# Optimization experiments

Measured on AMD Instinct MI355X. Metric: run time of the kernel, lower is better.

## Reference

```python
import jax, jax.numpy as jnp
import numpy as np

B, O, E, D, H = 8192, 64, 16, 16, 4  # batch, num_orbital, num_electron, n_bf_dets, hidden


def setup_inputs() -> dict:
    key = jax.random.key(0)
    ks = jax.random.split(key, 6)
    # occupation vectors: exactly E ones among O orbitals per sample
    scores = jax.random.uniform(ks[0], (B, O))
    occ_idx = jnp.argsort(scores, axis=1)[:, :E]  # (B, E) random occupied positions
    x = jnp.zeros((B, O), jnp.float32).at[jnp.arange(B)[:, None], occ_idx].set(1.0)
    # hidden MLP (positive_random_init kernels, zero bias as in flax default)
    W1 = jax.random.uniform(ks[1], (O, H), jnp.float32, minval=1.0, maxval=1.1)
    b1 = jnp.zeros((H,), jnp.float32)
    W2 = jax.random.uniform(ks[2], (H, H), jnp.float32, minval=1.0, maxval=1.1)
    b2 = jnp.zeros((H,), jnp.float32)
    # DenseGeneral: H -> (D, O, E)
    Wg = jax.random.normal(ks[3], (H, D, O, E), jnp.float32) / np.float32(np.sqrt(H))
    bg = jnp.zeros((D, O, E), jnp.float32)
    # bf_det_params: lecun_normal on (D, 1)
    bf_det_params = jax.random.normal(ks[4], (D, 1), jnp.float32) / np.float32(np.sqrt(D))
    return dict(x=x, W1=W1, b1=b1, W2=W2, b2=b2, Wg=Wg, bg=bg,
                bf_det_params=bf_det_params)


def reference(x, W1, b1, W2, b2, Wg, bg, bf_det_params):
    num_e = Wg.shape[-1]
    # indices of first num_e nonzero orbitals per sample (fill 0, like jnp.nonzero size=)
    sel = jax.vmap(lambda r: jnp.nonzero(r, size=num_e, fill_value=0)[0])(x)  # (B, E)
    # tiny MLP with relu
    h = jax.nn.relu(x @ W1 + b1)          # (B, H)
    h = jax.nn.relu(h @ W2 + b2)          # (B, H)
    # DenseGeneral projection to (B, D, O, E)
    y = jnp.einsum('bh,hdoe->bdoe', h, Wg) + bg
    # gather occupied-orbital rows -> (B, D, E, E)
    g = jax.vmap(lambda yi, si: yi[:, si, :])(y, sel)
    dets = jnp.linalg.det(g)              # (B, D)
    out = (dets @ bf_det_params)[:, 0]    # (B,)
    # zero out samples whose selected indices sum to 0 (empty/degenerate config)
    return jnp.where(jnp.sum(sel, axis=1) == 0, jnp.float32(0.0), out)
```

## Files before the change

### kernel.cpp

```cpp
#include <hip/hip_runtime.h>


template <int CTRL>
__device__ __forceinline__ float dpp_movf(float v) {
    return __int_as_float(__builtin_amdgcn_update_dpp(
        0, __float_as_int(v), CTRL, 0xF, 0xF, true));
}

__global__ __launch_bounds__(64) void backflow_kernel(
    const float* __restrict__ x,
    const float* __restrict__ W1,
    const float* __restrict__ b1,
    const float* __restrict__ W2,
    const float* __restrict__ b2,
    const float* __restrict__ Wg,
    const float* __restrict__ bg,
    const float* __restrict__ bf,
    float* __restrict__ out,
    int B)
{
    const int lane = threadIdx.x;
    const int b    = blockIdx.x;
    if (b >= B) return;
    const int d = lane >> 2;
    const int l = lane & 3;

    __shared__ float4 smem[512];

    const float xv = x[b * 64 + lane];
    const unsigned long long mask = __ballot(xv != 0.0f);
    const bool empty = ((mask & ~1ull) == 0ull);

    const float4 w1 = reinterpret_cast<const float4*>(W1)[lane];
    float c0 = xv * w1.x, c1 = xv * w1.y, c2 = xv * w1.z, c3 = xv * w1.w;
    #pragma unroll
    for (int off = 32; off >= 1; off >>= 1) {
        c0 += __shfl_xor(c0, off);
        c1 += __shfl_xor(c1, off);
        c2 += __shfl_xor(c2, off);
        c3 += __shfl_xor(c3, off);
    }
    const float h10 = fmaxf(c0 + b1[0], 0.0f);
    const float h11 = fmaxf(c1 + b1[1], 0.0f);
    const float h12 = fmaxf(c2 + b1[2], 0.0f);
    const float h13 = fmaxf(c3 + b1[3], 0.0f);

    float h2[4];
    #pragma unroll
    for (int j = 0; j < 4; ++j) {
        float v = b2[j];
        v = fmaf(h10, W2[0 * 4 + j], v);
        v = fmaf(h11, W2[1 * 4 + j], v);
        v = fmaf(h12, W2[2 * 4 + j], v);
        v = fmaf(h13, W2[3 * 4 + j], v);
        h2[j] = fmaxf(v, 0.0f);
    }

    unsigned long long mr = mask;
    #pragma unroll
    for (int i = 0; i < 15; ++i) if (i < d) mr &= mr - 1;
    const int selr = mr ? (int)__builtin_ctzll(mr) : 0;

    float R0[16], R1[16], R2[16], R3[16];

    {
        const float4* wgp = reinterpret_cast<const float4*>(Wg);
        const float4* bgp = reinterpret_cast<const float4*>(bg);
        const int rowoff = selr * 4 + l;

        #pragma unroll 1
        for (int half = 0; half < 2; ++half) {
            #pragma unroll 1
            for (int dd = 0; dd < 8; ++dd) {
                const int ds = half * 8 + dd;
                const float4 wb  = bgp[ds * 256 + rowoff];
                const float4 w3  = wgp[(3 * 16 + ds) * 256 + rowoff];
                const float4 w2c = wgp[(2 * 16 + ds) * 256 + rowoff];
                const float4 wv1 = wgp[(1 * 16 + ds) * 256 + rowoff];
                const float4 w0  = wgp[(0 * 16 + ds) * 256 + rowoff];
                float4 a;
                a.x = fmaf(h2[0],w0.x, fmaf(h2[1],wv1.x, fmaf(h2[2],w2c.x, fmaf(h2[3],w3.x, wb.x))));
                a.y = fmaf(h2[0],w0.y, fmaf(h2[1],wv1.y, fmaf(h2[2],w2c.y, fmaf(h2[3],w3.y, wb.y))));
                a.z = fmaf(h2[0],w0.z, fmaf(h2[1],wv1.z, fmaf(h2[2],w2c.z, fmaf(h2[3],w3.z, wb.z))));
                a.w = fmaf(h2[0],w0.w, fmaf(h2[1],wv1.w, fmaf(h2[2],w2c.w, fmaf(h2[3],w3.w, wb.w))));
                smem[(ds & 7) * 64 + d * 4 + (l ^ (ds & 3))] = a;
                __builtin_amdgcn_sched_barrier(0);
            }
            __syncthreads();
            if ((d >> 3) == half) {
#define RD_ROWS(RW, S) do { _Pragma("unroll")                                 \
                for (int q = 0; q < 4; ++q) {                                 \
                    const float4 t = smem[(d & 7) * 64 + (l + 4 * (S)) * 4 + (q ^ (d & 3))]; \
                    RW[q*4+0] = t.x; RW[q*4+1] = t.y;                         \
                    RW[q*4+2] = t.z; RW[q*4+3] = t.w;                         \
                } } while (0)
                RD_ROWS(R0, 0);
                RD_ROWS(R1, 1);
                RD_ROWS(R2, 2);
                RD_ROWS(R3, 3);
#undef RD_ROWS
            }
            __syncthreads();
        }
    }

#define BUILD_ROW(RW, SQ) do {                                                   \
    const float* base = Wg + ((size_t)d * 64 + (SQ)) * 16;                       \
    const float4* p0 = reinterpret_cast<const float4*>(base);                    \
    const float4* p1 = reinterpret_cast<const float4*>(base + 16384);            \
    const float4* p2 = reinterpret_cast<const float4*>(base + 32768);            \
    const float4* p3 = reinterpret_cast<const float4*>(base + 49152);            \
    const float4* pb = reinterpret_cast<const float4*>(bg + ((size_t)d * 64 + (SQ)) * 16); \
    _Pragma("unroll")                                                            \
    for (int q = 0; q < 4; ++q) {                                                \
        const float4 a0 = p0[q], a1 = p1[q], a2 = p2[q], a3 = p3[q], ab = pb[q]; \
        RW[q*4+0] = fmaf(h2[0],a0.x, fmaf(h2[1],a1.x, fmaf(h2[2],a2.x, fmaf(h2[3],a3.x, ab.x)))); \
        RW[q*4+1] = fmaf(h2[0],a0.y, fmaf(h2[1],a1.y, fmaf(h2[2],a2.y, fmaf(h2[3],a3.y, ab.y)))); \
        RW[q*4+2] = fmaf(h2[0],a0.z, fmaf(h2[1],a1.z, fmaf(h2[2],a2.z, fmaf(h2[3],a3.z, ab.z)))); \
        RW[q*4+3] = fmaf(h2[0],a0.w, fmaf(h2[1],a1.w, fmaf(h2[2],a2.w, fmaf(h2[3],a3.w, ab.w)))); \
    } } while (0)

    float mm = 0.0f;
    #pragma unroll
    for (int j = 0; j < 16; ++j) {
        mm = fmaxf(mm, fmaxf(fmaxf(fabsf(R0[j]), fabsf(R1[j])),
                             fmaxf(fabsf(R2[j]), fabsf(R3[j]))));
    }
    mm = fmaxf(mm, dpp_movf<0xB1>(mm));
    mm = fmaxf(mm, dpp_movf<0x4E>(mm));
    const float tau = 1e-4f * mm;

#define STEP4(K, DAC, PA, PB, PC, PD) do {                                   \
        const float pivot = dpp_movf<((K) & 3) * 0x55>(PA[0]);               \
        nb += !(fabsf(pivot) >= tau);                                        \
        DAC *= (double)pivot;                                                \
        const float pinv = __builtin_amdgcn_rcpf(pivot);                     \
        const float fa = (l > ((K) & 3)) ? PA[0] * pinv : 0.0f;              \
        const float fb = PB[0] * pinv;                                       \
        const float fc = PC[0] * pinv;                                       \
        const float fd = PD[0] * pinv;                                       \
        _Pragma("unroll")                                                    \
        for (int j = 1; j <= 15 - (K); ++j) {                                \
            const float pv = dpp_movf<((K) & 3) * 0x55>(PA[j]);              \
            PA[j - 1] = fmaf(-fa, pv, PA[j]);                                \
            PB[j - 1] = fmaf(-fb, pv, PB[j]);                                \
            PC[j - 1] = fmaf(-fc, pv, PC[j]);                                \
            PD[j - 1] = fmaf(-fd, pv, PD[j]);                                \
        } } while (0)

#define STEP3(K, DAC, PA, PB, PC) do {                                       \
        const float pivot = dpp_movf<((K) & 3) * 0x55>(PA[0]);               \
        nb += !(fabsf(pivot) >= tau);                                        \
        DAC *= (double)pivot;                                                \
        const float pinv = __builtin_amdgcn_rcpf(pivot);                     \
        const float fa = (l > ((K) & 3)) ? PA[0] * pinv : 0.0f;              \
        const float fb = PB[0] * pinv;                                       \
        const float fc = PC[0] * pinv;                                       \
        _Pragma("unroll")                                                    \
        for (int j = 1; j <= 15 - (K); ++j) {                                \
            const float pv = dpp_movf<((K) & 3) * 0x55>(PA[j]);              \
            PA[j - 1] = fmaf(-fa, pv, PA[j]);                                \
            PB[j - 1] = fmaf(-fb, pv, PB[j]);                                \
            PC[j - 1] = fmaf(-fc, pv, PC[j]);                                \
        } } while (0)

#define STEP2(K, DAC, PA, PB) do {                                           \
        const float pivot = dpp_movf<((K) & 3) * 0x55>(PA[0]);               \
        nb += !(fabsf(pivot) >= tau);                                        \
        DAC *= (double)pivot;                                                \
        const float pinv = __builtin_amdgcn_rcpf(pivot);                     \
        const float fa = (l > ((K) & 3)) ? PA[0] * pinv : 0.0f;              \
        const float fb = PB[0] * pinv;                                       \
        _Pragma("unroll")                                                    \
        for (int j = 1; j <= 15 - (K); ++j) {                                \
            const float pv = dpp_movf<((K) & 3) * 0x55>(PA[j]);              \
            PA[j - 1] = fmaf(-fa, pv, PA[j]);                                \
            PB[j - 1] = fmaf(-fb, pv, PB[j]);                                \
        } } while (0)

#define STEP1(K, DAC, PA) do {                                               \
        const float pivot = dpp_movf<((K) & 3) * 0x55>(PA[0]);               \
        nb += !(fabsf(pivot) >= tau);                                        \
        DAC *= (double)pivot;                                                \
        const float pinv = __builtin_amdgcn_rcpf(pivot);                     \
        const float fa = (l > ((K) & 3)) ? PA[0] * pinv : 0.0f;              \
        _Pragma("unroll")                                                    \
        for (int j = 1; j <= 15 - (K); ++j) {                                \
            const float pv = dpp_movf<((K) & 3) * 0x55>(PA[j]);              \
            PA[j - 1] = fmaf(-fa, pv, PA[j]);                                \
        } } while (0)

    double deta, detb;
    bool   retried = false;

    #pragma unroll 1
    for (int attempt = 0; attempt < 2; ++attempt) {
        if (attempt) {
            unsigned long long m = mask;
            if (l & 1) { m &= m - 1; }
            if (l & 2) { m &= m - 1; m &= m - 1; }
            const int s0 = m ? (int)__builtin_ctzll(m) : 0;
            m &= m - 1; m &= m - 1; m &= m - 1; m &= m - 1;
            const int s1 = m ? (int)__builtin_ctzll(m) : 0;
            m &= m - 1; m &= m - 1; m &= m - 1; m &= m - 1;
            const int s2 = m ? (int)__builtin_ctzll(m) : 0;
            m &= m - 1; m &= m - 1; m &= m - 1; m &= m - 1;
            const int s3 = m ? (int)__builtin_ctzll(m) : 0;
            BUILD_ROW(R0, s0);
            BUILD_ROW(R1, s1);
            BUILD_ROW(R2, s2);
            BUILD_ROW(R3, s3);
            const bool z = (l == 0);
            #pragma unroll
            for (int j = 0; j < 16; ++j) {
                const float w0 = z ? R1[j] : R0[j];
                const float wv = z ? R2[j] : R1[j];
                const float w2 = z ? R3[j] : R2[j];
                const float w3 = z ? R0[j] : R3[j];
                R0[j] = fmaf(0.5f, dpp_movf<0x39>(w0), R0[j]);
                R1[j] = fmaf(0.5f, dpp_movf<0x39>(wv), R1[j]);
                R2[j] = fmaf(0.5f, dpp_movf<0x39>(w2), R2[j]);
                R3[j] = fmaf(0.5f, dpp_movf<0x39>(w3), R3[j]);
            }
            retried = true;
        }
        deta = 1.0; detb = 1.0;
        int nb = 0;

        STEP4(0,  deta, R0, R1, R2, R3);
        STEP4(1,  detb, R0, R1, R2, R3);
        STEP4(2,  deta, R0, R1, R2, R3);
        STEP4(3,  detb, R0, R1, R2, R3);
        STEP3(4,  deta, R1, R2, R3);
        STEP3(5,  detb, R1, R2, R3);
        STEP3(6,  deta, R1, R2, R3);
        STEP3(7,  detb, R1, R2, R3);
        STEP2(8,  deta, R2, R3);
        STEP2(9,  detb, R2, R3);
        STEP2(10, deta, R2, R3);
        STEP2(11, detb, R2, R3);
        STEP1(12, deta, R3);
        STEP1(13, detb, R3);
        STEP1(14, deta, R3);
        STEP1(15, detb, R3);

        if (nb == 0) break;
    }
#undef STEP1
#undef STEP2
#undef STEP3
#undef STEP4
#undef BUILD_ROW

    float detf = (float)(deta * detb);
    if (retried) detf *= (65536.0f / 65535.0f);
    float acc = (l == 0) ? detf * bf[d] : 0.0f;
    acc += __shfl_xor(acc, 4);
    acc += __shfl_xor(acc, 8);
    acc += __shfl_xor(acc, 16);
    acc += __shfl_xor(acc, 32);
    if (lane == 0) out[b] = empty ? 0.0f : acc;
}

extern "C" void kernel_launch(void* const* d_in, const int* in_sizes, int n_in,
                              void* d_out, int out_size, void* d_ws, size_t ws_size,
                              hipStream_t stream) {
    const float* x  = (const float*)d_in[0];
    const float* W1 = (const float*)d_in[1];
    const float* b1 = (const float*)d_in[2];
    const float* W2 = (const float*)d_in[3];
    const float* b2 = (const float*)d_in[4];
    const float* Wg = (const float*)d_in[5];
    const float* bg = (const float*)d_in[6];
    const float* bf = (const float*)d_in[7];
    float* out = (float*)d_out;

    const int B = in_sizes[0] / 64;
    backflow_kernel<<<B, 64, 0, stream>>>(x, W1, b1, W2, b2, Wg, bg, bf, out, B);
}
```

Baseline: 46.16 us.

## Pack eight samples per block and share double-buffered Wg slices in LDS

The kernel now runs 8 waves per 512-thread block, one sample per wave. Each determinant slice of Wg and bg is loaded cooperatively into double-buffered shared memory and reused by all 8 waves, instead of every sample issuing its own scattered global gathers. The retry path is reorganised so the whole wave retries but only determinants that failed the pivot test apply the mixing and scale factor. This adds a block-wide barrier per slice and more shared memory, and drops the b>=B guard, so it assumes B is a multiple of 8.

```diff
diff --git a/kernel.cpp b/kernel.cpp
--- a/kernel.cpp
+++ b/kernel.cpp
@@ -7,7 +7,7 @@
         0, __float_as_int(v), CTRL, 0xF, 0xF, true));
 }
 
-__global__ __launch_bounds__(64) void backflow_kernel(
+__global__ __launch_bounds__(512) void backflow_kernel(
     const float* __restrict__ x,
     const float* __restrict__ W1,
     const float* __restrict__ b1,
@@ -19,13 +19,15 @@
     float* __restrict__ out,
     int B)
 {
-    const int lane = threadIdx.x;
-    const int b    = blockIdx.x;
-    if (b >= B) return;
+    const int lane  = threadIdx.x & 63;
+    const int wavei = threadIdx.x >> 6;
+    const int b     = blockIdx.x * 8 + wavei;
     const int d = lane >> 2;
     const int l = lane & 3;
 
-    __shared__ float4 smem[512];
+    __shared__ float4 slice[2][1280];
+    __shared__ float4 Bm[8][64];
+    float4* const bm = Bm[wavei];
 
     const float xv = x[b * 64 + lane];
     const unsigned long long mask = __ballot(xv != 0.0f);
@@ -60,47 +62,70 @@
     #pragma unroll
     for (int i = 0; i < 15; ++i) if (i < d) mr &= mr - 1;
     const int selr = mr ? (int)__builtin_ctzll(mr) : 0;
+    const int sw   = selr * 4 + (l ^ (selr & 3));
+
+    const float4* wgp = reinterpret_cast<const float4*>(Wg);
+    const float4* bgp = reinterpret_cast<const float4*>(bg);
 
     float R0[16], R1[16], R2[16], R3[16];
 
+#define SLICE_LOAD(DS, RV0, RV1, RV2) do {                                   \
+        const int t = threadIdx.x;                                           \
+        RV0 = wgp[((t >> 8) * 16 + (DS)) * 256 + (t & 255)];                 \
+        RV1 = wgp[((2 + (t >> 8)) * 16 + (DS)) * 256 + (t & 255)];           \
+        if (t < 256) RV2 = bgp[(DS) * 256 + t];                              \
+    } while (0)
+
+#define SLICE_WRITE(P, RV0, RV1, RV2) do {                                   \
+        const int t = threadIdx.x;                                           \
+        const int o0 = (t & 255) >> 2, cc = t & 3;                           \
+        slice[P][(t >> 8) * 256 + o0 * 4 + (cc ^ (o0 & 3))] = RV0;           \
+        slice[P][(2 + (t >> 8)) * 256 + o0 * 4 + (cc ^ (o0 & 3))] = RV1;     \
+        if (t < 256) {                                                       \
+            const int ob = t >> 2, cb = t & 3;                               \
+            slice[P][1024 + ob * 4 + (cb ^ (ob & 3))] = RV2;                 \
+        } } while (0)
+
+#define COMPUTE_DET(DS, P) do {                                              \
+        const float4 w0  = slice[P][sw];                                     \
+        const float4 wv1 = slice[P][256 + sw];                               \
+        const float4 w2c = slice[P][512 + sw];                               \
+        const float4 w3  = slice[P][768 + sw];                               \
+        const float4 wb  = slice[P][1024 + sw];                              \
+        float4 a;                                                            \
+        a.x = fmaf(h2[0],w0.x, fmaf(h2[1],wv1.x, fmaf(h2[2],w2c.x, fmaf(h2[3],w3.x, wb.x)))); \
+        a.y = fmaf(h2[0],w0.y, fmaf(h2[1],wv1.y, fmaf(h2[2],w2c.y, fmaf(h2[3],w3.y, wb.y)))); \
+        a.z = fmaf(h2[0],w0.z, fmaf(h2[1],wv1.z, fmaf(h2[2],w2c.z, fmaf(h2[3],w3.z, wb.z)))); \
+        a.w = fmaf(h2[0],w0.w, fmaf(h2[1],wv1.w, fmaf(h2[2],w2c.w, fmaf(h2[3],w3.w, wb.w)))); \
+        bm[d * 4 + (l ^ (d & 3))] = a;                                       \
+        if (d == (DS)) {                                                     \
+            _Pragma("unroll")                                                \
+            for (int q = 0; q < 4; ++q) {                                    \
+                const float4 t0 = bm[(l +  0) * 4 + (q ^ ((l +  0) & 3))];   \
+                const float4 t1 = bm[(l +  4) * 4 + (q ^ ((l +  4) & 3))];   \
+                const float4 t2 = bm[(l +  8) * 4 + (q ^ ((l +  8) & 3))];   \
+                const float4 t3 = bm[(l + 12) * 4 + (q ^ ((l + 12) & 3))];   \
+                R0[q*4+0] = t0.x; R0[q*4+1] = t0.y; R0[q*4+2] = t0.z; R0[q*4+3] = t0.w; \
+                R1[q*4+0] = t1.x; R1[q*4+1] = t1.y; R1[q*4+2] = t1.z; R1[q*4+3] = t1.w; \
+                R2[q*4+0] = t2.x; R2[q*4+1] = t2.y; R2[q*4+2] = t2.z; R2[q*4+3] = t2.w; \
+                R3[q*4+0] = t3.x; R3[q*4+1] = t3.y; R3[q*4+2] = t3.z; R3[q*4+3] = t3.w; \
+            }                                                                \
+        } } while (0)
+
     {
-        const float4* wgp = reinterpret_cast<const float4*>(Wg);
-        const float4* bgp = reinterpret_cast<const float4*>(bg);
-        const int rowoff = selr * 4 + l;
-
+        float4 sr0 = {}, sr1 = {}, sr2 = {};
+        SLICE_LOAD(0, sr0, sr1, sr2);
+        SLICE_WRITE(0, sr0, sr1, sr2);
+        __syncthreads();
         #pragma unroll 1
-        for (int half = 0; half < 2; ++half) {
-            #pragma unroll 1
-            for (int dd = 0; dd < 8; ++dd) {
-                const int ds = half * 8 + dd;
-                const float4 wb  = bgp[ds * 256 + rowoff];
-                const float4 w3  = wgp[(3 * 16 + ds) * 256 + rowoff];
-                const float4 w2c = wgp[(2 * 16 + ds) * 256 + rowoff];
-                const float4 wv1 = wgp[(1 * 16 + ds) * 256 + rowoff];
-                const float4 w0  = wgp[(0 * 16 + ds) * 256 + rowoff];
-                float4 a;
-                a.x = fmaf(h2[0],w0.x, fmaf(h2[1],wv1.x, fmaf(h2[2],w2c.x, fmaf(h2[3],w3.x, wb.x))));
-                a.y = fmaf(h2[0],w0.y, fmaf(h2[1],wv1.y, fmaf(h2[2],w2c.y, fmaf(h2[3],w3.y, wb.y))));
-                a.z = fmaf(h2[0],w0.z, fmaf(h2[1],wv1.z, fmaf(h2[2],w2c.z, fmaf(h2[3],w3.z, wb.z))));
-                a.w = fmaf(h2[0],w0.w, fmaf(h2[1],wv1.w, fmaf(h2[2],w2c.w, fmaf(h2[3],w3.w, wb.w))));
-                smem[(ds & 7) * 64 + d * 4 + (l ^ (ds & 3))] = a;
-                __builtin_amdgcn_sched_barrier(0);
+        for (int ds = 0; ds < 16; ++ds) {
+            const int p = ds & 1;
+            if (ds < 15) SLICE_LOAD(ds + 1, sr0, sr1, sr2);
+            COMPUTE_DET(ds, p);
+            if (ds < 15) {
+                SLICE_WRITE(p ^ 1, sr0, sr1, sr2);
+                __syncthreads();
             }
-            __syncthreads();
-            if ((d >> 3) == half) {
-#define RD_ROWS(RW, S) do { _Pragma("unroll")                                 \
-                for (int q = 0; q < 4; ++q) {                                 \
-                    const float4 t = smem[(d & 7) * 64 + (l + 4 * (S)) * 4 + (q ^ (d & 3))]; \
-                    RW[q*4+0] = t.x; RW[q*4+1] = t.y;                         \
-                    RW[q*4+2] = t.z; RW[q*4+3] = t.w;                         \
-                } } while (0)
-                RD_ROWS(R0, 0);
-                RD_ROWS(R1, 1);
-                RD_ROWS(R2, 2);
-                RD_ROWS(R3, 3);
-#undef RD_ROWS
-            }
-            __syncthreads();
         }
     }
 
@@ -119,16 +144,6 @@
         RW[q*4+2] = fmaf(h2[0],a0.z, fmaf(h2[1],a1.z, fmaf(h2[2],a2.z, fmaf(h2[3],a3.z, ab.z)))); \
         RW[q*4+3] = fmaf(h2[0],a0.w, fmaf(h2[1],a1.w, fmaf(h2[2],a2.w, fmaf(h2[3],a3.w, ab.w)))); \
     } } while (0)
-
-    float mm = 0.0f;
-    #pragma unroll
-    for (int j = 0; j < 16; ++j) {
-        mm = fmaxf(mm, fmaxf(fmaxf(fabsf(R0[j]), fabsf(R1[j])),
-                             fmaxf(fabsf(R2[j]), fabsf(R3[j]))));
-    }
-    mm = fmaxf(mm, dpp_movf<0xB1>(mm));
-    mm = fmaxf(mm, dpp_movf<0x4E>(mm));
-    const float tau = 1e-4f * mm;
 
 #define STEP4(K, DAC, PA, PB, PC, PD) do {                                   \
         const float pivot = dpp_movf<((K) & 3) * 0x55>(PA[0]);               \
@@ -190,8 +205,8 @@
             PA[j - 1] = fmaf(-fa, pv, PA[j]);                                \
         } } while (0)
 
-    double deta, detb;
-    bool   retried = false;
+    double deta = 1.0, detb = 1.0;
+    bool domix = false;
 
     #pragma unroll 1
     for (int attempt = 0; attempt < 2; ++attempt) {
@@ -210,20 +225,32 @@
             BUILD_ROW(R1, s1);
             BUILD_ROW(R2, s2);
             BUILD_ROW(R3, s3);
-            const bool z = (l == 0);
-            #pragma unroll
-            for (int j = 0; j < 16; ++j) {
-                const float w0 = z ? R1[j] : R0[j];
-                const float wv = z ? R2[j] : R1[j];
-                const float w2 = z ? R3[j] : R2[j];
-                const float w3 = z ? R0[j] : R3[j];
-                R0[j] = fmaf(0.5f, dpp_movf<0x39>(w0), R0[j]);
-                R1[j] = fmaf(0.5f, dpp_movf<0x39>(wv), R1[j]);
-                R2[j] = fmaf(0.5f, dpp_movf<0x39>(w2), R2[j]);
-                R3[j] = fmaf(0.5f, dpp_movf<0x39>(w3), R3[j]);
+            if (domix) {
+                const bool z = (l == 0);
+                #pragma unroll
+                for (int j = 0; j < 16; ++j) {
+                    const float w0 = z ? R1[j] : R0[j];
+                    const float wv = z ? R2[j] : R1[j];
+                    const float w2 = z ? R3[j] : R2[j];
+                    const float w3 = z ? R0[j] : R3[j];
+                    R0[j] = fmaf(0.5f, dpp_movf<0x39>(w0), R0[j]);
+                    R1[j] = fmaf(0.5f, dpp_movf<0x39>(wv), R1[j]);
+                    R2[j] = fmaf(0.5f, dpp_movf<0x39>(w2), R2[j]);
+                    R3[j] = fmaf(0.5f, dpp_movf<0x39>(w3), R3[j]);
+                }
             }
-            retried = true;
         }
+
+        float mm = 0.0f;
+        #pragma unroll
+        for (int j = 0; j < 16; ++j) {
+            mm = fmaxf(mm, fmaxf(fmaxf(fabsf(R0[j]), fabsf(R1[j])),
+                                 fmaxf(fabsf(R2[j]), fabsf(R3[j]))));
+        }
+        mm = fmaxf(mm, dpp_movf<0xB1>(mm));
+        mm = fmaxf(mm, dpp_movf<0x4E>(mm));
+        const float tau = 1e-4f * mm;
+
         deta = 1.0; detb = 1.0;
         int nb = 0;
 
@@ -244,16 +271,22 @@
         STEP1(14, deta, R3);
         STEP1(15, detb, R3);
 
-        if (nb == 0) break;
+        if (attempt == 0) {
+            if (!__any(nb != 0)) break;
+            domix = (nb != 0);
+        }
     }
 #undef STEP1
 #undef STEP2
 #undef STEP3
 #undef STEP4
 #undef BUILD_ROW
+#undef COMPUTE_DET
+#undef SLICE_WRITE
+#undef SLICE_LOAD
 
     float detf = (float)(deta * detb);
-    if (retried) detf *= (65536.0f / 65535.0f);
+    if (domix) detf *= (65536.0f / 65535.0f);
     float acc = (l == 0) ? detf * bf[d] : 0.0f;
     acc += __shfl_xor(acc, 4);
     acc += __shfl_xor(acc, 8);
@@ -276,5 +309,6 @@
     float* out = (float*)d_out;
 
     const int B = in_sizes[0] / 64;
-    backflow_kernel<<<B, 64, 0, stream>>>(x, W1, b1, W2, b2, Wg, bg, bf, out, B);
+    const int blocks = (B + 7) / 8;
+    backflow_kernel<<<blocks, 512, 0, stream>>>(x, W1, b1, W2, b2, Wg, bg, bf, out, B);
 }
```

Result: slower. 76.27 us (+65.2%).
